# Performance work log

Hardware: AMD Instinct MI355X
Metric: run time of the kernel (lower is better)

Reference implementation:

```python
import jax, jax.numpy as jnp
import numpy as np

B, S, H, A, F, NCATE, VOCAB, EMB, NCONT = 64, 1024, 512, 256, 2048, 4, 1000, 64, 4


def _layernorm(x, g, b, eps=1e-5):
    m = jnp.mean(x, axis=-1, keepdims=True)
    v = jnp.mean((x - m) ** 2, axis=-1, keepdims=True)
    return (x - m) * jax.lax.rsqrt(v + eps) * g + b


def _positional_encoding(seq_len, d, base=10000.0):
    pos = jnp.arange(seq_len, dtype=jnp.float32)[:, None]
    i = jnp.arange(0, d, 2, dtype=jnp.float32)[None, :]
    ang = pos / jnp.power(base, i / d)
    pe = jnp.zeros((seq_len, d), dtype=jnp.float32)
    pe = pe.at[:, 0::2].set(jnp.sin(ang))
    pe = pe.at[:, 1::2].set(jnp.cos(ang))
    return pe


def setup_inputs() -> dict:
    key = jax.random.key(0)
    ks = jax.random.split(key, 24)
    s = lambda i, shape, fan: jax.random.normal(ks[i], shape, jnp.float32) / np.sqrt(fan)
    inp = {
        'cate_x': jax.random.randint(ks[0], (B, S, NCATE), 0, VOCAB, jnp.int32),
        'cont_x': jax.random.normal(ks[1], (B, S, NCONT), jnp.float32),
        'mask': (jax.random.uniform(ks[2], (B, S)) < 0.9).astype(jnp.float32),
        'targets': jax.random.uniform(ks[3], (B, S), jnp.float32),
        'E_cate': s(4, (NCATE, VOCAB, EMB), EMB),
        'W_proj': s(5, (NCATE * EMB + NCONT, H), NCATE * EMB + NCONT),
        'WQ1': s(6, (H, A), H), 'WK1': s(7, (H, A), H), 'WV1': s(8, (H, A), H),
        'WQ2': s(9, (H, A), H), 'WK2': s(10, (H, A), H), 'WV2': s(11, (H, A), H),
        'W0': s(12, (2 * A, H), 2 * A),
        'ln1_g': jnp.ones((H,), jnp.float32), 'ln1_b': jnp.zeros((H,), jnp.float32),
        'Wf1': s(13, (H, F), H), 'bf1': jnp.zeros((F,), jnp.float32),
        'Wf2': s(14, (F, H), F), 'bf2': jnp.zeros((H,), jnp.float32),
        'ln2_g': jnp.ones((H,), jnp.float32), 'ln2_b': jnp.zeros((H,), jnp.float32),
        'Wfin': s(15, (H, 1), H), 'bfin': jnp.zeros((1,), jnp.float32),
    }
    return inp


def _attn_branch(x, WQ, WK, WV, mask_bias):
    Q = x @ WQ  # [B,S,A]
    K = x @ WK
    V = x @ WV
    scores = jnp.einsum('bsa,bta->bst', Q, K) / np.sqrt(A)
    scores = scores + mask_bias  # additive key-mask [B,1,S]
    return jnp.einsum('bst,bta->bsa', jax.nn.softmax(scores, axis=-1), V)


def reference(cate_x, cont_x, mask, targets, E_cate, W_proj, WQ1, WK1, WV1,
              WQ2, WK2, WV2, W0, ln1_g, ln1_b, Wf1, bf1, Wf2, bf2, ln2_g,
              ln2_b, Wfin, bfin):
    # embedding: per-feature lookup, concat with continuous, project to hidden
    emb = jax.vmap(lambda tab, idx: tab[idx], in_axes=(0, 2), out_axes=2)(E_cate, cate_x)
    emb = emb.reshape(B, S, NCATE * EMB)
    x = jnp.concatenate([emb, cont_x], axis=-1) @ W_proj  # [B,S,H]
    x = x + _positional_encoding(S, H)[None]
    mask_bias = (mask * 1e6 - 1e6)[:, None, :]  # [B,1,S]
    z1 = _attn_branch(x, WQ1, WK1, WV1, mask_bias)
    z2 = _attn_branch(x, WQ2, WK2, WV2, mask_bias)
    z = jnp.concatenate([z1, z2], axis=-1) @ W0
    z = _layernorm(x + z, ln1_g, ln1_b)
    fz = jax.nn.relu(z @ Wf1 + bf1) @ Wf2 + bf2
    z3 = _layernorm(z + fz, ln2_g, ln2_b)
    out = (z3 @ Wfin + bfin).squeeze(-1)  # [B,S]
    return out
```

## Files before the change

kernel.cpp:

```cpp
#include <hip/hip_runtime.h>

typedef unsigned short ushort_t;
typedef unsigned int uint32;
typedef float f32x4 __attribute__((ext_vector_type(4)));
typedef short bf16x8 __attribute__((ext_vector_type(8)));

__device__ __forceinline__ float bf2f(short u) {
  union { uint32 u32; float f; } cv;
  cv.u32 = ((uint32)(ushort_t)u) << 16;
  return cv.f;
}
__device__ __forceinline__ ushort_t f2bf(float f) {
  union { float f; uint32 u; } cv; cv.f = f;
  return (ushort_t)((cv.u + 0x7fffu + ((cv.u >> 16) & 1u)) >> 16);
}
__device__ __forceinline__ uint32 pack2bf(float lo, float hi) {
  return (uint32)f2bf(lo) | ((uint32)f2bf(hi) << 16);
}
__device__ __forceinline__ f32x4 mfma16(bf16x8 a, bf16x8 b, f32x4 c) {
  return __builtin_amdgcn_mfma_f32_16x16x32_bf16(a, b, c, 0, 0, 0);
}
__device__ __forceinline__ void gld_lds16(const ushort_t* g, ushort_t* l) {
  __builtin_amdgcn_global_load_lds(
      (const __attribute__((address_space(1))) void*)g,
      (__attribute__((address_space(3))) void*)l, 16, 0, 0);
}

__global__ __launch_bounds__(256)
void transpose_w(const float* __restrict__ W, ushort_t* __restrict__ WT, int K, int N) {
  __shared__ float s[32][33];
  const int tx = threadIdx.x & 31, ty = threadIdx.x >> 5;
  const int k0 = blockIdx.x * 32, n0 = blockIdx.y * 32;
#pragma unroll
  for (int i = 0; i < 4; ++i)
    s[ty + i * 8][tx] = W[(size_t)(k0 + ty + i * 8) * N + n0 + tx];
  __syncthreads();
#pragma unroll
  for (int i = 0; i < 4; ++i)
    WT[(size_t)(n0 + ty + i * 8) * K + k0 + tx] = f2bf(s[tx][ty + i * 8]);
}

__global__ __launch_bounds__(256)
void ep_kernel(const float* __restrict__ E, const float* __restrict__ Wp,
               ushort_t* __restrict__ EP) {
  const int cv = blockIdx.x;
  const int c = cv / 1000;
  __shared__ float se[64];
  if (threadIdx.x < 64) se[threadIdx.x] = E[(size_t)cv * 64 + threadIdx.x];
  __syncthreads();
  const float* wrow = Wp + (size_t)c * 64 * 512;
  for (int h = threadIdx.x; h < 512; h += 256) {
    float acc = 0.f;
#pragma unroll
    for (int e = 0; e < 64; ++e) acc += se[e] * wrow[(size_t)e * 512 + h];
    EP[(size_t)cv * 512 + h] = f2bf(acc);
  }
}

__global__ __launch_bounds__(256)
void pe_kernel(float* __restrict__ PE) {
  const int id = blockIdx.x * 256 + threadIdx.x;
  const int s = id >> 8, i = id & 255;
  const float ang = (float)s * exp2f(-(float)i * (13.287712379549449f / 256.0f));
  PE[(size_t)s * 512 + 2 * i] = sinf(ang);
  PE[(size_t)s * 512 + 2 * i + 1] = cosf(ang);
}

__global__ __launch_bounds__(256)
void x_kernel(const int* __restrict__ cate, const float* __restrict__ cont,
              const float* __restrict__ Wp, const ushort_t* __restrict__ EP,
              const float* __restrict__ PE, ushort_t* __restrict__ X) {
  const int tid = threadIdx.x;
  const size_t r = (size_t)blockIdx.x * 4 + (tid >> 6);
  const int lane = tid & 63;
  const int h0 = lane * 8;
  const int s = (int)(r & 1023);
  float acc[8];
  const float4 p0 = *(const float4*)(PE + (size_t)s * 512 + h0);
  const float4 p1 = *(const float4*)(PE + (size_t)s * 512 + h0 + 4);
  acc[0] = p0.x; acc[1] = p0.y; acc[2] = p0.z; acc[3] = p0.w;
  acc[4] = p1.x; acc[5] = p1.y; acc[6] = p1.z; acc[7] = p1.w;
#pragma unroll
  for (int c = 0; c < 4; ++c) {
    const int idx = cate[r * 4 + c];
    const bf16x8 e8 = *(const bf16x8*)(EP + ((size_t)(c * 1000 + idx)) * 512 + h0);
#pragma unroll
    for (int k = 0; k < 8; ++k) acc[k] += bf2f(e8[k]);
  }
#pragma unroll
  for (int j = 0; j < 4; ++j) {
    const float cj = cont[r * 4 + j];
    const float4 w0 = *(const float4*)(Wp + (size_t)(256 + j) * 512 + h0);
    const float4 w1 = *(const float4*)(Wp + (size_t)(256 + j) * 512 + h0 + 4);
    acc[0] += cj * w0.x; acc[1] += cj * w0.y; acc[2] += cj * w0.z; acc[3] += cj * w0.w;
    acc[4] += cj * w1.x; acc[5] += cj * w1.y; acc[6] += cj * w1.z; acc[7] += cj * w1.w;
  }
  bf16x8 ov;
#pragma unroll
  for (int k = 0; k < 8; ++k) ov[k] = (short)f2bf(acc[k]);
  *(bf16x8*)(X + r * 512 + h0) = ov;
}

template <int EPI, bool TSTORE>
__global__ __launch_bounds__(256, 2)
void gemm_bt(const ushort_t* __restrict__ A, const ushort_t* __restrict__ BT,
             ushort_t* __restrict__ C, const float* __restrict__ bias, int N, int K) {
  __shared__ __align__(16) ushort_t sA[128 * 64];
  __shared__ __align__(16) ushort_t sB[128 * 64];
  const int tid = threadIdx.x;
  const int lane = tid & 63;
  const int wid = tid >> 6;
  const int l15 = lane & 15, l4 = lane >> 4;
  const int wr = (wid >> 1) * 64, wc = (wid & 1) * 64;
  const size_t rowA0 = (size_t)blockIdx.x * 128;
  const size_t rowB0 = (size_t)blockIdx.y * 128;

  f32x4 acc[4][4] = {};

  for (int kt = 0; kt < K; kt += 64) {
#pragma unroll
    for (int it = 0; it < 4; ++it) {
      const int L = it * 256 + tid;
      const int row = L >> 3;
      const int c = (L & 7) ^ (row & 7);
      gld_lds16(A + (rowA0 + row) * K + kt + c * 8, sA + (size_t)L * 8);
      gld_lds16(BT + (rowB0 + row) * K + kt + c * 8, sB + (size_t)L * 8);
    }
    __syncthreads();
#pragma unroll
    for (int kk = 0; kk < 2; ++kk) {
      bf16x8 af[4], bfr[4];
#pragma unroll
      for (int mi = 0; mi < 4; ++mi) {
        const int row = wr + mi * 16 + l15;
        const int c = (kk * 4 + l4) ^ (row & 7);
        af[mi] = *(const bf16x8*)(sA + row * 64 + c * 8);
      }
#pragma unroll
      for (int ni = 0; ni < 4; ++ni) {
        const int row = wc + ni * 16 + l15;
        const int c = (kk * 4 + l4) ^ (row & 7);
        bfr[ni] = *(const bf16x8*)(sB + row * 64 + c * 8);
      }
#pragma unroll
      for (int mi = 0; mi < 4; ++mi)
#pragma unroll
        for (int ni = 0; ni < 4; ++ni)
          acc[mi][ni] = mfma16(af[mi], bfr[ni], acc[mi][ni]);
    }
    __syncthreads();
  }
#pragma unroll
  for (int ni = 0; ni < 4; ++ni) {
    const int col = (int)rowB0 + wc + ni * 16 + l15;
    float bv = 0.f;
    if (EPI > 0) bv = bias[col];
#pragma unroll
    for (int mi = 0; mi < 4; ++mi) {
      const size_t row0 = rowA0 + wr + mi * 16 + l4 * 4;
      if (TSTORE) {
        ushort4 ov;
        ov.x = f2bf(acc[mi][ni][0]);
        ov.y = f2bf(acc[mi][ni][1]);
        ov.z = f2bf(acc[mi][ni][2]);
        ov.w = f2bf(acc[mi][ni][3]);
        *(ushort4*)(C + ((row0 >> 10) * 256 + (size_t)col) * 1024 + (row0 & 1023)) = ov;
      } else {
#pragma unroll
        for (int j = 0; j < 4; ++j) {
          float v = acc[mi][ni][j] + bv;
          if (EPI == 2) v = fmaxf(v, 0.f);
          C[(row0 + j) * N + col] = f2bf(v);
        }
      }
    }
  }
}

__global__ __launch_bounds__(256, 2)
void attn_kernel(const ushort_t* __restrict__ Q, const ushort_t* __restrict__ Kb,
                 const ushort_t* __restrict__ VT, const float* __restrict__ mask,
                 ushort_t* __restrict__ Z, int colOff) {
  __shared__ __align__(16) ushort_t sK[64 * 256];
  __shared__ __align__(16) ushort_t sV[256 * 64];
  const int tid = threadIdx.x, lane = tid & 63, w = tid >> 6;
  const int l15 = lane & 15, l4 = lane >> 4;
  const int b = blockIdx.y;
  const int q0 = blockIdx.x * 64 + w * 16;

  bf16x8 qf[8];
  {
    const ushort_t* qrow = Q + ((size_t)b * 1024 + q0 + l15) * 256;
#pragma unroll
    for (int kk = 0; kk < 8; ++kk)
      qf[kk] = *(const bf16x8*)(qrow + kk * 32 + l4 * 8);
  }
  float m_run = -3.0e38f, l_run = 0.f;
  f32x4 o[16] = {};
  const int src0 = ((l4 & 1) << 5) + l15;
  const bool hiSel = (l4 >= 2);

  for (int t0 = 0; t0 < 1024; t0 += 64) {
#pragma unroll
    for (int it = 0; it < 8; ++it) {
      const int L = it * 256 + tid;
      const int rk = L >> 5;
      const int ck = (L & 24) | ((L ^ rk) & 7);
      gld_lds16(Kb + ((size_t)b * 1024 + t0 + rk) * 256 + ck * 8, sK + (size_t)L * 8);
      const int rv = L >> 3;
      const int cv2 = (L ^ rv) & 7;
      gld_lds16(VT + ((size_t)b * 256 + rv) * 1024 + t0 + cv2 * 8, sV + (size_t)L * 8);
    }
    __syncthreads();

    f32x4 st[4] = {};
#pragma unroll
    for (int fi = 0; fi < 4; ++fi) {
      const int row = fi * 16 + l15;
      const ushort_t* kr = sK + row * 256;
#pragma unroll
      for (int kk = 0; kk < 8; ++kk) {
        const int c = kk * 4 + l4;
        const int cs = (c & 24) | ((c ^ row) & 7);
        const bf16x8 kf = *(const bf16x8*)(kr + cs * 8);
        st[fi] = mfma16(kf, qf[kk], st[fi]);
      }
    }

    float pr[4][4];
    float tmax = -3.0e38f;
#pragma unroll
    for (int fi = 0; fi < 4; ++fi) {
      const float4 mk = *(const float4*)(mask + (size_t)b * 1024 + t0 + fi * 16 + l4 * 4);
      pr[fi][0] = st[fi][0] * 0.0625f + (mk.x * 1e6f - 1e6f);
      pr[fi][1] = st[fi][1] * 0.0625f + (mk.y * 1e6f - 1e6f);
      pr[fi][2] = st[fi][2] * 0.0625f + (mk.z * 1e6f - 1e6f);
      pr[fi][3] = st[fi][3] * 0.0625f + (mk.w * 1e6f - 1e6f);
      tmax = fmaxf(tmax, fmaxf(fmaxf(pr[fi][0], pr[fi][1]), fmaxf(pr[fi][2], pr[fi][3])));
    }
    tmax = fmaxf(tmax, __shfl_xor(tmax, 16));
    tmax = fmaxf(tmax, __shfl_xor(tmax, 32));
    const float m_new = fmaxf(m_run, tmax);
    const float alpha = __expf(m_run - m_new);
    float rs = 0.f;
#pragma unroll
    for (int fi = 0; fi < 4; ++fi)
#pragma unroll
      for (int j = 0; j < 4; ++j) {
        pr[fi][j] = __expf(pr[fi][j] - m_new);
        rs += pr[fi][j];
      }
    rs += __shfl_xor(rs, 16);
    rs += __shfl_xor(rs, 32);
    l_run = l_run * alpha + rs;
    m_run = m_new;
#pragma unroll
    for (int ai = 0; ai < 16; ++ai) o[ai] *= alpha;

    uint32 pk[4][2];
#pragma unroll
    for (int fi = 0; fi < 4; ++fi) {
      pk[fi][0] = pack2bf(pr[fi][0], pr[fi][1]);
      pk[fi][1] = pack2bf(pr[fi][2], pr[fi][3]);
    }
    bf16x8 pf[2];
#pragma unroll
    for (int kk2 = 0; kk2 < 2; ++kk2) {
      const uint32 a0 = __shfl(pk[2 * kk2][0], src0);
      const uint32 a1 = __shfl(pk[2 * kk2][1], src0);
      const uint32 a2 = __shfl(pk[2 * kk2][0], src0 + 16);
      const uint32 a3 = __shfl(pk[2 * kk2][1], src0 + 16);
      const uint32 b0 = __shfl(pk[2 * kk2 + 1][0], src0);
      const uint32 b1 = __shfl(pk[2 * kk2 + 1][1], src0);
      const uint32 b2 = __shfl(pk[2 * kk2 + 1][0], src0 + 16);
      const uint32 b3 = __shfl(pk[2 * kk2 + 1][1], src0 + 16);
      uint4 wv;
      wv.x = hiSel ? b0 : a0;
      wv.y = hiSel ? b1 : a1;
      wv.z = hiSel ? b2 : a2;
      wv.w = hiSel ? b3 : a3;
      pf[kk2] = __builtin_bit_cast(bf16x8, wv);
    }

#pragma unroll
    for (int ai = 0; ai < 16; ++ai) {
      const int row = ai * 16 + l15;
      const ushort_t* vr = sV + row * 64;
#pragma unroll
      for (int kk2 = 0; kk2 < 2; ++kk2) {
        const int c = (kk2 * 4 + l4) ^ (row & 7);
        const bf16x8 vf = *(const bf16x8*)(vr + c * 8);
        o[ai] = mfma16(vf, pf[kk2], o[ai]);
      }
    }
    __syncthreads();
  }

  const float inv = 1.f / l_run;
  const size_t zrow = ((size_t)b * 1024 + q0 + l15) * 512;
#pragma unroll
  for (int ai = 0; ai < 16; ++ai) {
    ushort4 ov;
    ov.x = f2bf(o[ai][0] * inv);
    ov.y = f2bf(o[ai][1] * inv);
    ov.z = f2bf(o[ai][2] * inv);
    ov.w = f2bf(o[ai][3] * inv);
    *(ushort4*)(Z + zrow + colOff + ai * 16 + l4 * 4) = ov;
  }
}

__global__ __launch_bounds__(256)
void ln_kernel(const ushort_t* __restrict__ Xa, const ushort_t* __restrict__ Xb2,
               const float* __restrict__ g, const float* __restrict__ bb,
               ushort_t* __restrict__ O) {
  const int tid = threadIdx.x;
  const size_t r = (size_t)blockIdx.x * 4 + (tid >> 6);
  const int lane = tid & 63;
  const int h0 = lane * 8;
  const bf16x8 va = *(const bf16x8*)(Xa + r * 512 + h0);
  const bf16x8 vb = *(const bf16x8*)(Xb2 + r * 512 + h0);
  float v[8], s1 = 0.f, s2 = 0.f;
#pragma unroll
  for (int k = 0; k < 8; ++k) {
    v[k] = bf2f(va[k]) + bf2f(vb[k]);
    s1 += v[k];
    s2 += v[k] * v[k];
  }
#pragma unroll
  for (int m = 1; m < 64; m <<= 1) {
    s1 += __shfl_xor(s1, m);
    s2 += __shfl_xor(s2, m);
  }
  const float mean = s1 * (1.f / 512.f);
  const float var = s2 * (1.f / 512.f) - mean * mean;
  const float rstd = rsqrtf(var + 1e-5f);
  const float4 g0 = *(const float4*)(g + h0);
  const float4 g1 = *(const float4*)(g + h0 + 4);
  const float4 b0 = *(const float4*)(bb + h0);
  const float4 b1 = *(const float4*)(bb + h0 + 4);
  const float gg[8] = {g0.x, g0.y, g0.z, g0.w, g1.x, g1.y, g1.z, g1.w};
  const float bbv[8] = {b0.x, b0.y, b0.z, b0.w, b1.x, b1.y, b1.z, b1.w};
  bf16x8 ov;
#pragma unroll
  for (int k = 0; k < 8; ++k)
    ov[k] = (short)f2bf((v[k] - mean) * rstd * gg[k] + bbv[k]);
  *(bf16x8*)(O + r * 512 + h0) = ov;
}

__global__ __launch_bounds__(256)
void ln_fin_kernel(const ushort_t* __restrict__ Xa, const ushort_t* __restrict__ Xb2,
                   const float* __restrict__ g, const float* __restrict__ bb,
                   const float* __restrict__ Wfin, const float* __restrict__ bfin,
                   float* __restrict__ out) {
  const int tid = threadIdx.x;
  const size_t r = (size_t)blockIdx.x * 4 + (tid >> 6);
  const int lane = tid & 63;
  const int h0 = lane * 8;
  const bf16x8 va = *(const bf16x8*)(Xa + r * 512 + h0);
  const bf16x8 vb = *(const bf16x8*)(Xb2 + r * 512 + h0);
  float v[8], s1 = 0.f, s2 = 0.f;
#pragma unroll
  for (int k = 0; k < 8; ++k) {
    v[k] = bf2f(va[k]) + bf2f(vb[k]);
    s1 += v[k];
    s2 += v[k] * v[k];
  }
#pragma unroll
  for (int m = 1; m < 64; m <<= 1) {
    s1 += __shfl_xor(s1, m);
    s2 += __shfl_xor(s2, m);
  }
  const float mean = s1 * (1.f / 512.f);
  const float var = s2 * (1.f / 512.f) - mean * mean;
  const float rstd = rsqrtf(var + 1e-5f);
  const float4 g0 = *(const float4*)(g + h0);
  const float4 g1 = *(const float4*)(g + h0 + 4);
  const float4 b0 = *(const float4*)(bb + h0);
  const float4 b1 = *(const float4*)(bb + h0 + 4);
  const float4 w0 = *(const float4*)(Wfin + h0);
  const float4 w1 = *(const float4*)(Wfin + h0 + 4);
  const float gg[8] = {g0.x, g0.y, g0.z, g0.w, g1.x, g1.y, g1.z, g1.w};
  const float bbv[8] = {b0.x, b0.y, b0.z, b0.w, b1.x, b1.y, b1.z, b1.w};
  const float ww[8] = {w0.x, w0.y, w0.z, w0.w, w1.x, w1.y, w1.z, w1.w};
  float dot = 0.f;
#pragma unroll
  for (int k = 0; k < 8; ++k)
    dot += ((v[k] - mean) * rstd * gg[k] + bbv[k]) * ww[k];
#pragma unroll
  for (int m = 1; m < 64; m <<= 1) dot += __shfl_xor(dot, m);
  if (lane == 0) out[r] = dot + bfin[0];
}

extern "C" void kernel_launch(void* const* d_in, const int* in_sizes, int n_in,
                              void* d_out, int out_size, void* d_ws, size_t ws_size,
                              hipStream_t stream) {
  (void)in_sizes; (void)n_in; (void)out_size; (void)ws_size;
  const int* cate   = (const int*)d_in[0];
  const float* cont = (const float*)d_in[1];
  const float* mask = (const float*)d_in[2];
  const float* E    = (const float*)d_in[4];
  const float* Wp   = (const float*)d_in[5];
  const float* WQ1  = (const float*)d_in[6];
  const float* WK1  = (const float*)d_in[7];
  const float* WV1  = (const float*)d_in[8];
  const float* WQ2  = (const float*)d_in[9];
  const float* WK2  = (const float*)d_in[10];
  const float* WV2  = (const float*)d_in[11];
  const float* W0   = (const float*)d_in[12];
  const float* ln1g = (const float*)d_in[13];
  const float* ln1b = (const float*)d_in[14];
  const float* Wf1  = (const float*)d_in[15];
  const float* bf1  = (const float*)d_in[16];
  const float* Wf2  = (const float*)d_in[17];
  const float* bf2  = (const float*)d_in[18];
  const float* ln2g = (const float*)d_in[19];
  const float* ln2b = (const float*)d_in[20];
  const float* Wfin = (const float*)d_in[21];
  const float* bfin = (const float*)d_in[22];
  float* out = (float*)d_out;
  char* ws = (char*)d_ws;

  const size_t MB = 1ull << 20;
  ushort_t* Xb  = (ushort_t*)(ws + 0);
  ushort_t* Qb  = (ushort_t*)(ws + 64 * MB);
  ushort_t* Kb  = (ushort_t*)(ws + 96 * MB);
  ushort_t* VTb = (ushort_t*)(ws + 128 * MB);
  ushort_t* Zb  = (ushort_t*)(ws + 160 * MB);
  ushort_t* T0b = (ushort_t*)(ws + 64 * MB);
  ushort_t* H1b = (ushort_t*)(ws + 128 * MB);
  ushort_t* Gb  = (ushort_t*)(ws + 0);
  ushort_t* T1b = (ushort_t*)(ws + 64 * MB);
  const size_t OW = 224 * MB;
  ushort_t* wq1t = (ushort_t*)(ws + OW + 0);
  ushort_t* wk1t = (ushort_t*)(ws + OW + 262144);
  ushort_t* wv1t = (ushort_t*)(ws + OW + 524288);
  ushort_t* wq2t = (ushort_t*)(ws + OW + 786432);
  ushort_t* wk2t = (ushort_t*)(ws + OW + 1048576);
  ushort_t* wv2t = (ushort_t*)(ws + OW + 1310720);
  ushort_t* w0t  = (ushort_t*)(ws + OW + 1572864);
  ushort_t* wf1t = (ushort_t*)(ws + OW + 2097152);
  ushort_t* wf2t = (ushort_t*)(ws + OW + 4194304);
  ushort_t* epb  = (ushort_t*)(ws + OW + 6291456);
  float*    peb  = (float*)   (ws + OW + 10485760);

  const dim3 blk(256);
  transpose_w<<<dim3(16, 8), blk, 0, stream>>>(WQ1, wq1t, 512, 256);
  transpose_w<<<dim3(16, 8), blk, 0, stream>>>(WK1, wk1t, 512, 256);
  transpose_w<<<dim3(16, 8), blk, 0, stream>>>(WV1, wv1t, 512, 256);
  transpose_w<<<dim3(16, 8), blk, 0, stream>>>(WQ2, wq2t, 512, 256);
  transpose_w<<<dim3(16, 8), blk, 0, stream>>>(WK2, wk2t, 512, 256);
  transpose_w<<<dim3(16, 8), blk, 0, stream>>>(WV2, wv2t, 512, 256);
  transpose_w<<<dim3(16, 16), blk, 0, stream>>>(W0, w0t, 512, 512);
  transpose_w<<<dim3(16, 64), blk, 0, stream>>>(Wf1, wf1t, 512, 2048);
  transpose_w<<<dim3(64, 16), blk, 0, stream>>>(Wf2, wf2t, 2048, 512);
  ep_kernel<<<4000, blk, 0, stream>>>(E, Wp, epb);
  pe_kernel<<<1024, blk, 0, stream>>>(peb);
  x_kernel<<<16384, blk, 0, stream>>>(cate, cont, Wp, epb, peb, Xb);
  gemm_bt<0, false><<<dim3(512, 2), blk, 0, stream>>>(Xb, wq1t, Qb, nullptr, 256, 512);
  gemm_bt<0, false><<<dim3(512, 2), blk, 0, stream>>>(Xb, wk1t, Kb, nullptr, 256, 512);
  gemm_bt<0, true><<<dim3(512, 2), blk, 0, stream>>>(Xb, wv1t, VTb, nullptr, 256, 512);
  attn_kernel<<<dim3(16, 64), blk, 0, stream>>>(Qb, Kb, VTb, mask, Zb, 0);
  gemm_bt<0, false><<<dim3(512, 2), blk, 0, stream>>>(Xb, wq2t, Qb, nullptr, 256, 512);
  gemm_bt<0, false><<<dim3(512, 2), blk, 0, stream>>>(Xb, wk2t, Kb, nullptr, 256, 512);
  gemm_bt<0, true><<<dim3(512, 2), blk, 0, stream>>>(Xb, wv2t, VTb, nullptr, 256, 512);
  attn_kernel<<<dim3(16, 64), blk, 0, stream>>>(Qb, Kb, VTb, mask, Zb, 256);
  gemm_bt<0, false><<<dim3(512, 4), blk, 0, stream>>>(Zb, w0t, T0b, nullptr, 512, 512);
  ln_kernel<<<16384, blk, 0, stream>>>(Xb, T0b, ln1g, ln1b, H1b);
  for (int rc = 0; rc < 4; ++rc) {
    const ushort_t* h1c = H1b + (size_t)rc * 16384 * 512;
    ushort_t* t1c = T1b + (size_t)rc * 16384 * 512;
    gemm_bt<2, false><<<dim3(128, 16), blk, 0, stream>>>(h1c, wf1t, Gb, bf1, 2048, 512);
    gemm_bt<1, false><<<dim3(128, 4), blk, 0, stream>>>(Gb, wf2t, t1c, bf2, 512, 2048);
  }
  ln_fin_kernel<<<16384, blk, 0, stream>>>(H1b, T1b, ln2g, ln2b, Wfin, bfin, out);
}
```

Baseline: 1.084 ms.

## Double-buffer GEMM LDS tiles and widen attention to 32 queries per wave

The GEMM kernel gets two LDS buffers so the next K-tile is loaded while the current one is computed, with one barrier per iteration instead of two. The attention kernel now handles 32 query rows per wave (128 per block), so each K/V tile in LDS is reused across twice as many queries. Its grid is remapped so the blocks of one batch share an XCD for L2 locality. A lazy-rescale softmax skips the rescaling of the output accumulators unless the running max rises by more than 8. The trade-off is double the GEMM LDS footprint and many more registers in attention, which may lower occupancy under launch_bounds(256,2).

```diff
diff --git a/kernel.cpp b/kernel.cpp
--- a/kernel.cpp
+++ b/kernel.cpp
@@ -105,8 +105,8 @@
 __global__ __launch_bounds__(256, 2)
 void gemm_bt(const ushort_t* __restrict__ A, const ushort_t* __restrict__ BT,
              ushort_t* __restrict__ C, const float* __restrict__ bias, int N, int K) {
-  __shared__ __align__(16) ushort_t sA[128 * 64];
-  __shared__ __align__(16) ushort_t sB[128 * 64];
+  __shared__ __align__(16) ushort_t sA[2][128 * 64];
+  __shared__ __align__(16) ushort_t sB[2][128 * 64];
   const int tid = threadIdx.x;
   const int lane = tid & 63;
   const int wid = tid >> 6;
@@ -117,16 +117,17 @@
 
   f32x4 acc[4][4] = {};
 
-  for (int kt = 0; kt < K; kt += 64) {
+  auto stage = [&](int buf, int kt) {
 #pragma unroll
     for (int it = 0; it < 4; ++it) {
       const int L = it * 256 + tid;
       const int row = L >> 3;
       const int c = (L & 7) ^ (row & 7);
-      gld_lds16(A + (rowA0 + row) * K + kt + c * 8, sA + (size_t)L * 8);
-      gld_lds16(BT + (rowB0 + row) * K + kt + c * 8, sB + (size_t)L * 8);
-    }
-    __syncthreads();
+      gld_lds16(A + (rowA0 + row) * K + kt + c * 8, sA[buf] + (size_t)L * 8);
+      gld_lds16(BT + (rowB0 + row) * K + kt + c * 8, sB[buf] + (size_t)L * 8);
+    }
+  };
+  auto compute = [&](int buf) {
 #pragma unroll
     for (int kk = 0; kk < 2; ++kk) {
       bf16x8 af[4], bfr[4];
@@ -134,13 +135,13 @@
       for (int mi = 0; mi < 4; ++mi) {
         const int row = wr + mi * 16 + l15;
         const int c = (kk * 4 + l4) ^ (row & 7);
-        af[mi] = *(const bf16x8*)(sA + row * 64 + c * 8);
+        af[mi] = *(const bf16x8*)(sA[buf] + row * 64 + c * 8);
       }
 #pragma unroll
       for (int ni = 0; ni < 4; ++ni) {
         const int row = wc + ni * 16 + l15;
         const int c = (kk * 4 + l4) ^ (row & 7);
-        bfr[ni] = *(const bf16x8*)(sB + row * 64 + c * 8);
+        bfr[ni] = *(const bf16x8*)(sB[buf] + row * 64 + c * 8);
       }
 #pragma unroll
       for (int mi = 0; mi < 4; ++mi)
@@ -148,8 +149,19 @@
         for (int ni = 0; ni < 4; ++ni)
           acc[mi][ni] = mfma16(af[mi], bfr[ni], acc[mi][ni]);
     }
+  };
+
+  stage(0, 0);
+  __syncthreads();
+  int cur = 0;
+  for (int kt = 64; kt < K; kt += 64) {
+    stage(cur ^ 1, kt);
+    compute(cur);
     __syncthreads();
-  }
+    cur ^= 1;
+  }
+  compute(cur);
+
 #pragma unroll
   for (int ni = 0; ni < 4; ++ni) {
     const int col = (int)rowB0 + wc + ni * 16 + l15;
@@ -185,18 +197,21 @@
   __shared__ __align__(16) ushort_t sV[256 * 64];
   const int tid = threadIdx.x, lane = tid & 63, w = tid >> 6;
   const int l15 = lane & 15, l4 = lane >> 4;
-  const int b = blockIdx.y;
-  const int q0 = blockIdx.x * 64 + w * 16;
-
-  bf16x8 qf[8];
-  {
-    const ushort_t* qrow = Q + ((size_t)b * 1024 + q0 + l15) * 256;
+  const int id = blockIdx.x;
+  const int xcd = id & 7, sub = id >> 3;
+  const int b = (xcd << 3) | (sub >> 3);
+  const int q0 = (sub & 7) * 128 + w * 32;
+
+  bf16x8 qf[2][8];
+#pragma unroll
+  for (int g = 0; g < 2; ++g) {
+    const ushort_t* qrow = Q + ((size_t)b * 1024 + q0 + g * 16 + l15) * 256;
 #pragma unroll
     for (int kk = 0; kk < 8; ++kk)
-      qf[kk] = *(const bf16x8*)(qrow + kk * 32 + l4 * 8);
-  }
-  float m_run = -3.0e38f, l_run = 0.f;
-  f32x4 o[16] = {};
+      qf[g][kk] = *(const bf16x8*)(qrow + kk * 32 + l4 * 8);
+  }
+  float m_run[2] = {-3.0e38f, -3.0e38f}, l_run[2] = {0.f, 0.f};
+  f32x4 o[2][16] = {};
   const int src0 = ((l4 & 1) << 5) + l15;
   const bool hiSel = (l4 >= 2);
 
@@ -213,7 +228,7 @@
     }
     __syncthreads();
 
-    f32x4 st[4] = {};
+    f32x4 st[2][4] = {};
 #pragma unroll
     for (int fi = 0; fi < 4; ++fi) {
       const int row = fi * 16 + l15;
@@ -223,63 +238,82 @@
         const int c = kk * 4 + l4;
         const int cs = (c & 24) | ((c ^ row) & 7);
         const bf16x8 kf = *(const bf16x8*)(kr + cs * 8);
-        st[fi] = mfma16(kf, qf[kk], st[fi]);
-      }
-    }
-
-    float pr[4][4];
-    float tmax = -3.0e38f;
+        st[0][fi] = mfma16(kf, qf[0][kk], st[0][fi]);
+        st[1][fi] = mfma16(kf, qf[1][kk], st[1][fi]);
+      }
+    }
+
+    float tmax0 = -3.0e38f, tmax1 = -3.0e38f;
 #pragma unroll
     for (int fi = 0; fi < 4; ++fi) {
       const float4 mk = *(const float4*)(mask + (size_t)b * 1024 + t0 + fi * 16 + l4 * 4);
-      pr[fi][0] = st[fi][0] * 0.0625f + (mk.x * 1e6f - 1e6f);
-      pr[fi][1] = st[fi][1] * 0.0625f + (mk.y * 1e6f - 1e6f);
-      pr[fi][2] = st[fi][2] * 0.0625f + (mk.z * 1e6f - 1e6f);
-      pr[fi][3] = st[fi][3] * 0.0625f + (mk.w * 1e6f - 1e6f);
-      tmax = fmaxf(tmax, fmaxf(fmaxf(pr[fi][0], pr[fi][1]), fmaxf(pr[fi][2], pr[fi][3])));
-    }
-    tmax = fmaxf(tmax, __shfl_xor(tmax, 16));
-    tmax = fmaxf(tmax, __shfl_xor(tmax, 32));
-    const float m_new = fmaxf(m_run, tmax);
-    const float alpha = __expf(m_run - m_new);
-    float rs = 0.f;
-#pragma unroll
-    for (int fi = 0; fi < 4; ++fi)
-#pragma unroll
-      for (int j = 0; j < 4; ++j) {
-        pr[fi][j] = __expf(pr[fi][j] - m_new);
-        rs += pr[fi][j];
-      }
-    rs += __shfl_xor(rs, 16);
-    rs += __shfl_xor(rs, 32);
-    l_run = l_run * alpha + rs;
-    m_run = m_new;
-#pragma unroll
-    for (int ai = 0; ai < 16; ++ai) o[ai] *= alpha;
-
-    uint32 pk[4][2];
-#pragma unroll
-    for (int fi = 0; fi < 4; ++fi) {
-      pk[fi][0] = pack2bf(pr[fi][0], pr[fi][1]);
-      pk[fi][1] = pack2bf(pr[fi][2], pr[fi][3]);
-    }
-    bf16x8 pf[2];
-#pragma unroll
-    for (int kk2 = 0; kk2 < 2; ++kk2) {
-      const uint32 a0 = __shfl(pk[2 * kk2][0], src0);
-      const uint32 a1 = __shfl(pk[2 * kk2][1], src0);
-      const uint32 a2 = __shfl(pk[2 * kk2][0], src0 + 16);
-      const uint32 a3 = __shfl(pk[2 * kk2][1], src0 + 16);
-      const uint32 b0 = __shfl(pk[2 * kk2 + 1][0], src0);
-      const uint32 b1 = __shfl(pk[2 * kk2 + 1][1], src0);
-      const uint32 b2 = __shfl(pk[2 * kk2 + 1][0], src0 + 16);
-      const uint32 b3 = __shfl(pk[2 * kk2 + 1][1], src0 + 16);
-      uint4 wv;
-      wv.x = hiSel ? b0 : a0;
-      wv.y = hiSel ? b1 : a1;
-      wv.z = hiSel ? b2 : a2;
-      wv.w = hiSel ? b3 : a3;
-      pf[kk2] = __builtin_bit_cast(bf16x8, wv);
+      const float mb0 = mk.x * 1e6f - 1e6f, mb1 = mk.y * 1e6f - 1e6f;
+      const float mb2 = mk.z * 1e6f - 1e6f, mb3 = mk.w * 1e6f - 1e6f;
+      st[0][fi][0] = st[0][fi][0] * 0.0625f + mb0;
+      st[0][fi][1] = st[0][fi][1] * 0.0625f + mb1;
+      st[0][fi][2] = st[0][fi][2] * 0.0625f + mb2;
+      st[0][fi][3] = st[0][fi][3] * 0.0625f + mb3;
+      st[1][fi][0] = st[1][fi][0] * 0.0625f + mb0;
+      st[1][fi][1] = st[1][fi][1] * 0.0625f + mb1;
+      st[1][fi][2] = st[1][fi][2] * 0.0625f + mb2;
+      st[1][fi][3] = st[1][fi][3] * 0.0625f + mb3;
+      tmax0 = fmaxf(tmax0, fmaxf(fmaxf(st[0][fi][0], st[0][fi][1]),
+                                 fmaxf(st[0][fi][2], st[0][fi][3])));
+      tmax1 = fmaxf(tmax1, fmaxf(fmaxf(st[1][fi][0], st[1][fi][1]),
+                                 fmaxf(st[1][fi][2], st[1][fi][3])));
+    }
+    tmax0 = fmaxf(tmax0, __shfl_xor(tmax0, 16));
+    tmax0 = fmaxf(tmax0, __shfl_xor(tmax0, 32));
+    tmax1 = fmaxf(tmax1, __shfl_xor(tmax1, 16));
+    tmax1 = fmaxf(tmax1, __shfl_xor(tmax1, 32));
+
+    const bool ok = (tmax0 <= m_run[0] + 8.f) && (tmax1 <= m_run[1] + 8.f);
+    if (!__all(ok)) {
+      const float mn0 = fmaxf(m_run[0], tmax0);
+      const float mn1 = fmaxf(m_run[1], tmax1);
+      const float a0 = __expf(m_run[0] - mn0);
+      const float a1 = __expf(m_run[1] - mn1);
+      l_run[0] *= a0; l_run[1] *= a1;
+      m_run[0] = mn0; m_run[1] = mn1;
+#pragma unroll
+      for (int ai = 0; ai < 16; ++ai) { o[0][ai] *= a0; o[1][ai] *= a1; }
+    }
+
+    bf16x8 pf[2][2];
+#pragma unroll
+    for (int g = 0; g < 2; ++g) {
+      float rs = 0.f;
+      uint32 pk[4][2];
+#pragma unroll
+      for (int fi = 0; fi < 4; ++fi) {
+        const float p0 = __expf(st[g][fi][0] - m_run[g]);
+        const float p1 = __expf(st[g][fi][1] - m_run[g]);
+        const float p2 = __expf(st[g][fi][2] - m_run[g]);
+        const float p3 = __expf(st[g][fi][3] - m_run[g]);
+        rs += (p0 + p1) + (p2 + p3);
+        pk[fi][0] = pack2bf(p0, p1);
+        pk[fi][1] = pack2bf(p2, p3);
+      }
+      rs += __shfl_xor(rs, 16);
+      rs += __shfl_xor(rs, 32);
+      l_run[g] += rs;
+#pragma unroll
+      for (int kk2 = 0; kk2 < 2; ++kk2) {
+        const uint32 a0v = __shfl(pk[2 * kk2][0], src0);
+        const uint32 a1v = __shfl(pk[2 * kk2][1], src0);
+        const uint32 a2v = __shfl(pk[2 * kk2][0], src0 + 16);
+        const uint32 a3v = __shfl(pk[2 * kk2][1], src0 + 16);
+        const uint32 b0v = __shfl(pk[2 * kk2 + 1][0], src0);
+        const uint32 b1v = __shfl(pk[2 * kk2 + 1][1], src0);
+        const uint32 b2v = __shfl(pk[2 * kk2 + 1][0], src0 + 16);
+        const uint32 b3v = __shfl(pk[2 * kk2 + 1][1], src0 + 16);
+        uint4 wv;
+        wv.x = hiSel ? b0v : a0v;
+        wv.y = hiSel ? b1v : a1v;
+        wv.z = hiSel ? b2v : a2v;
+        wv.w = hiSel ? b3v : a3v;
+        pf[g][kk2] = __builtin_bit_cast(bf16x8, wv);
+      }
     }
 
 #pragma unroll
@@ -290,22 +324,26 @@
       for (int kk2 = 0; kk2 < 2; ++kk2) {
         const int c = (kk2 * 4 + l4) ^ (row & 7);
         const bf16x8 vf = *(const bf16x8*)(vr + c * 8);
-        o[ai] = mfma16(vf, pf[kk2], o[ai]);
+        o[0][ai] = mfma16(vf, pf[0][kk2], o[0][ai]);
+        o[1][ai] = mfma16(vf, pf[1][kk2], o[1][ai]);
       }
     }
     __syncthreads();
   }
 
-  const float inv = 1.f / l_run;
-  const size_t zrow = ((size_t)b * 1024 + q0 + l15) * 512;
-#pragma unroll
-  for (int ai = 0; ai < 16; ++ai) {
-    ushort4 ov;
-    ov.x = f2bf(o[ai][0] * inv);
-    ov.y = f2bf(o[ai][1] * inv);
-    ov.z = f2bf(o[ai][2] * inv);
-    ov.w = f2bf(o[ai][3] * inv);
-    *(ushort4*)(Z + zrow + colOff + ai * 16 + l4 * 4) = ov;
+#pragma unroll
+  for (int g = 0; g < 2; ++g) {
+    const float inv = 1.f / l_run[g];
+    const size_t zrow = ((size_t)b * 1024 + q0 + g * 16 + l15) * 512;
+#pragma unroll
+    for (int ai = 0; ai < 16; ++ai) {
+      ushort4 ov;
+      ov.x = f2bf(o[g][ai][0] * inv);
+      ov.y = f2bf(o[g][ai][1] * inv);
+      ov.z = f2bf(o[g][ai][2] * inv);
+      ov.w = f2bf(o[g][ai][3] * inv);
+      *(ushort4*)(Z + zrow + colOff + ai * 16 + l4 * 4) = ov;
+    }
   }
 }
 
@@ -459,11 +497,11 @@
   gemm_bt<0, false><<<dim3(512, 2), blk, 0, stream>>>(Xb, wq1t, Qb, nullptr, 256, 512);
   gemm_bt<0, false><<<dim3(512, 2), blk, 0, stream>>>(Xb, wk1t, Kb, nullptr, 256, 512);
   gemm_bt<0, true><<<dim3(512, 2), blk, 0, stream>>>(Xb, wv1t, VTb, nullptr, 256, 512);
-  attn_kernel<<<dim3(16, 64), blk, 0, stream>>>(Qb, Kb, VTb, mask, Zb, 0);
+  attn_kernel<<<dim3(512), blk, 0, stream>>>(Qb, Kb, VTb, mask, Zb, 0);
   gemm_bt<0, false><<<dim3(512, 2), blk, 0, stream>>>(Xb, wq2t, Qb, nullptr, 256, 512);
   gemm_bt<0, false><<<dim3(512, 2), blk, 0, stream>>>(Xb, wk2t, Kb, nullptr, 256, 512);
   gemm_bt<0, true><<<dim3(512, 2), blk, 0, stream>>>(Xb, wv2t, VTb, nullptr, 256, 512);
-  attn_kernel<<<dim3(16, 64), blk, 0, stream>>>(Qb, Kb, VTb, mask, Zb, 256);
+  attn_kernel<<<dim3(512), blk, 0, stream>>>(Qb, Kb, VTb, mask, Zb, 256);
   gemm_bt<0, false><<<dim3(512, 4), blk, 0, stream>>>(Zb, w0t, T0b, nullptr, 512, 512);
   ln_kernel<<<16384, blk, 0, stream>>>(Xb, T0b, ln1g, ln1b, H1b);
   for (int rc = 0; rc < 4; ++rc) {
```

After: 1.271 ms. 17.3% more time.
